# Performance work log

Hardware: AMD Instinct MI355X
Metric: run time of the kernel (lower is better)

## Reference

```python
import jax, jax.numpy as jnp
import numpy as np

B, S, H = 8, 2048, 1024
NEG = 1.0e10


def setup_inputs() -> dict:
    key = jax.random.key(0)
    ks = jax.random.split(key, 9)
    scale = 1.0 / np.sqrt(H)
    x = jax.random.normal(ks[0], (B, S, H), dtype=jnp.float32)
    Wq = jax.random.normal(ks[1], (H, H), dtype=jnp.float32) * scale
    bq = jnp.zeros((H,), dtype=jnp.float32)
    Wk = jax.random.normal(ks[2], (H, H), dtype=jnp.float32) * scale
    bk = jnp.zeros((H,), dtype=jnp.float32)
    Wv = jax.random.normal(ks[3], (H, H), dtype=jnp.float32) * scale
    bv = jnp.zeros((H,), dtype=jnp.float32)
    gamma = jnp.ones((H,), dtype=jnp.float32)
    beta = jnp.zeros((H,), dtype=jnp.float32)
    return {"x": x, "Wq": Wq, "bq": bq, "Wk": Wk, "bk": bk,
            "Wv": Wv, "bv": bv, "gamma": gamma, "beta": beta}


def _layernorm(y, gamma, beta, eps=1e-5):
    mu = jnp.mean(y, axis=-1, keepdims=True)
    var = jnp.var(y, axis=-1, keepdims=True)
    return (y - mu) * jax.lax.rsqrt(var + eps) * gamma + beta


def reference(x, Wq, bq, Wk, bk, Wv, bv, gamma, beta):
    # QKV projections (single head, no 1/sqrt(d) scaling, per original code)
    q = x @ Wq + bq                       # [B, S, H]
    k = x @ Wk + bk                       # [B, S, H]
    v = x @ Wv + bv                       # [B, S, H]
    scores = jnp.einsum('bsh,bth->bst', q, k)   # [B, S, S]
    # non-standard multiplicative-subtractive causal mask
    mask = jnp.tril(jnp.ones((S, S), dtype=scores.dtype))  # [S, S]
    scores = scores * mask - NEG * (1.0 - mask)
    probs = jax.nn.softmax(scores, axis=-1)
    attn = jnp.einsum('bst,bth->bsh', probs, v)
    return _layernorm(v + attn, gamma, beta)
```

## Files before the change

### kernel.cpp

```cpp
#include <hip/hip_runtime.h>

#define SQ 2048
#define HD 1024
#define NB 8
#define NTOT (NB*SQ)
#define NT2 8
#define NTRI2 36
#define CE ((long long)NTRI2*65536)

typedef _Float16 f16x8 __attribute__((ext_vector_type(8)));
typedef float f32x4 __attribute__((ext_vector_type(4)));
typedef short s16x8 __attribute__((ext_vector_type(8)));
typedef unsigned short u16;

__device__ __forceinline__ u16 f2h(float x){
  _Float16 h = (_Float16)x;
  u16 u; __builtin_memcpy(&u, &h, 2); return u;
}

#define STG(gp, lp) __builtin_amdgcn_global_load_lds( \
    (const __attribute__((address_space(1))) unsigned*)(gp), \
    (__attribute__((address_space(3))) unsigned*)(lp), 16, 0, 0)

template<int EPI>
__global__ __launch_bounds__(512, 2)
void gemm8(const u16* __restrict__ A, const u16* __restrict__ B,
           float* Cf, u16* Ch, u16* Vt,
           const float* __restrict__ b0, const float* __restrict__ b1,
           const float* __restrict__ b2,
           int K, int lda, int ldb, int ldc,
           long long sA, long long sB, long long sC)
{
  const int z = blockIdx.z;
  int bi, bj, tri = 0;
  if (EPI == 1){
    int t = blockIdx.x;
    int i = (int)((sqrtf(8.f * (float)t + 1.f) - 1.f) * 0.5f);
    while ((i + 1) * (i + 2) / 2 <= t) ++i;
    while (i * (i + 1) / 2 > t) --i;
    bi = i;  bj = t - i * (i + 1) / 2;  tri = t;
  } else {
    bi = blockIdx.x;  bj = blockIdx.y;
    if (EPI == 2) tri = bi * (bi + 1) / 2;
  }

  __shared__ short lds[4 * 16384];

  const int tid  = threadIdx.x;
  const int lane = tid & 63, w = tid >> 6;
  const int wm2 = w >> 2, wn4 = w & 3;
  const int lrow = lane & 15, kgrp = lane >> 4;

  const long long rowA = (long long)bi * 256;
  const long long colB = (long long)bj * 256;

  const int rt = tid >> 3;
  const int qp = (tid & 7) ^ (rt & 7);
  const int kq = qp & 3;
  const int rh = (qp >> 2) << 7;

  const u16 *sAp[2], *sBp[2];
  if (EPI == 2){
    const u16* Pb = A + (long long)z * sA + (long long)tri * 65536;
    #pragma unroll
    for (int i = 0; i < 2; i++)
      sAp[i] = Pb + (i * 64 + rt + rh) * 256 + kq * 8;
  } else {
    const u16* Ab = A + (EPI == 0 ? 0LL : (long long)z * sA);
    #pragma unroll
    for (int i = 0; i < 2; i++)
      sAp[i] = Ab + (rowA + i * 64 + rt + rh) * (long long)lda + kq * 8;
  }
  {
    const u16* Bb = B + (long long)z * sB;
    #pragma unroll
    for (int i = 0; i < 2; i++)
      sBp[i] = Bb + (colB + i * 64 + rt + rh) * (long long)ldb + kq * 8;
  }

  const int aoff = lrow * 64 + ((((wm2 << 2) | kgrp) ^ (lrow & 7)) << 3);
  const int boff = 8192 + ((wn4 & 1) * 64 + lrow) * 64
                 + (((((wn4 >> 1) << 2) | kgrp) ^ (lrow & 7)) << 3);

  f32x4 acc[8][4];
  const f32x4 zf = {0.f, 0.f, 0.f, 0.f};
  #pragma unroll
  for (int m = 0; m < 8; m++)
    #pragma unroll
    for (int n = 0; n < 4; n++) acc[m][n] = zf;

  int KT = K >> 5;
  if (EPI == 2){ int t = (bi + 1) * 8; if (t < KT) KT = t; }

  auto stage = [&](int b){
    #pragma unroll
    for (int i = 0; i < 2; i++) STG(sAp[i], lds + b * 16384 +        (i * 8 + w) * 512);
    #pragma unroll
    for (int i = 0; i < 2; i++) STG(sBp[i], lds + b * 16384 + 8192 + (i * 8 + w) * 512);
  };
  auto advance = [&](int tS){
    long long advA = 32;
    if (EPI == 2) advA = ((tS & 7) == 7) ? (65536 - 224) : 32;
    sAp[0] += advA; sAp[1] += advA; sBp[0] += 32; sBp[1] += 32;
  };

  stage(0); advance(0);
  if (KT > 1){ stage(1); advance(1); }
  if (KT > 2){ stage(2); advance(2); }
  if (KT > 2)      { asm volatile("s_waitcnt vmcnt(8)" ::: "memory"); }
  else if (KT > 1) { asm volatile("s_waitcnt vmcnt(4)" ::: "memory"); }
  else             { asm volatile("s_waitcnt vmcnt(0)" ::: "memory"); }
  __builtin_amdgcn_s_barrier();

  for (int kt = 0; kt < KT; ++kt){
    const short* Ab = lds + (kt & 3) * 16384;
    if (kt + 3 < KT){ stage((kt + 3) & 3); advance(kt + 3); }

    f16x8 bfr[4], af[4];
    #pragma unroll
    for (int n = 0; n < 4; n++)
      bfr[n] = *(const f16x8*)(Ab + boff + n * 1024);
    #pragma unroll
    for (int m = 0; m < 4; m++)
      af[m] = *(const f16x8*)(Ab + aoff + m * 1024);

    __builtin_amdgcn_s_setprio(1);
    #pragma unroll
    for (int n = 0; n < 4; n++)
      #pragma unroll
      for (int m = 0; m < 4; m++)
        acc[m][n] = __builtin_amdgcn_mfma_f32_16x16x32_f16(af[m], bfr[n], acc[m][n], 0, 0, 0);
    __builtin_amdgcn_s_setprio(0);
    __builtin_amdgcn_s_barrier();

    #pragma unroll
    for (int m = 0; m < 4; m++)
      af[m] = *(const f16x8*)(Ab + aoff + (4 + m) * 1024);

    __builtin_amdgcn_s_setprio(1);
    #pragma unroll
    for (int n = 0; n < 4; n++)
      #pragma unroll
      for (int m = 0; m < 4; m++)
        acc[4 + m][n] = __builtin_amdgcn_mfma_f32_16x16x32_f16(af[m], bfr[n], acc[4 + m][n], 0, 0, 0);
    __builtin_amdgcn_s_setprio(0);

    const int rem = KT - 1 - kt;
    if (rem >= 3)      { asm volatile("s_waitcnt vmcnt(8)" ::: "memory"); }
    else if (rem == 2) { asm volatile("s_waitcnt vmcnt(4)" ::: "memory"); }
    else if (rem == 1) { asm volatile("s_waitcnt vmcnt(0)" ::: "memory"); }
    if (rem > 0) __builtin_amdgcn_s_barrier();
  }

  if (EPI == 0){
    if (z < 2){
      u16* c = Ch + (long long)z * sC;
      const float* bias = z ? b1 : b0;
      #pragma unroll
      for (int n = 0; n < 4; n++){
        int col = (int)colB + wn4 * 64 + n * 16 + lrow;
        float ba = bias[col];
        #pragma unroll
        for (int m = 0; m < 8; m++){
          long long r = rowA + wm2 * 128 + m * 16 + kgrp * 4;
          #pragma unroll
          for (int j = 0; j < 4; j++)
            c[(r + j) * ldc + col] = f2h(acc[m][n][j] + ba);
        }
      }
    } else {
      #pragma unroll
      for (int n = 0; n < 4; n++){
        int col = (int)colB + wn4 * 64 + n * 16 + lrow;
        float ba = b2[col];
        #pragma unroll
        for (int m = 0; m < 8; m++){
          long long r = rowA + wm2 * 128 + m * 16 + kgrp * 4;
          int bb = (int)(r >> 11);
          int s  = (int)(r & 2047);
          u16* vtc = Vt + ((long long)bb * HD + col) * SQ + s;
          #pragma unroll
          for (int j = 0; j < 4; j++){
            float v = acc[m][n][j] + ba;
            Cf[(r + j) * ldc + col] = v;
            vtc[j] = f2h(v);
          }
        }
      }
    }
  } else if (EPI == 1){
    float* cf = Cf + (long long)z * sC + (long long)tri * 65536;
    #pragma unroll
    for (int n = 0; n < 4; n++){
      int col = wn4 * 64 + n * 16 + lrow;
      #pragma unroll
      for (int m = 0; m < 8; m++){
        int r = wm2 * 128 + m * 16 + kgrp * 4;
        #pragma unroll
        for (int j = 0; j < 4; j++)
          cf[(r + j) * 256 + col] = acc[m][n][j];
      }
    }
  } else {
    float* cf = Cf + (long long)z * sC;
    #pragma unroll
    for (int n = 0; n < 4; n++){
      int col = (int)colB + wn4 * 64 + n * 16 + lrow;
      #pragma unroll
      for (int m = 0; m < 8; m++){
        long long r = rowA + wm2 * 128 + m * 16 + kgrp * 4;
        #pragma unroll
        for (int j = 0; j < 4; j++){
          long long o = (r + j) * ldc + col;
          cf[o] = acc[m][n][j] + cf[o];
        }
      }
    }
  }
}

__global__ __launch_bounds__(256)
void prep_x(const float* __restrict__ X, u16* __restrict__ Xh)
{
  const long long n8 = (long long)NTOT * HD / 8;
  for (long long i = (long long)blockIdx.x * 256 + threadIdx.x; i < n8;
       i += (long long)gridDim.x * 256){
    const float* p = X + i * 8;
    float4 a = *(const float4*)p;
    float4 b = *(const float4*)(p + 4);
    float f[8] = {a.x, a.y, a.z, a.w, b.x, b.y, b.z, b.w};
    s16x8 h;
    #pragma unroll
    for (int j = 0; j < 8; j++) h[j] = (short)f2h(f[j]);
    *(s16x8*)&Xh[i * 8] = h;
  }
}

__global__ void prep_w(const float* __restrict__ Wq, const float* __restrict__ Wk,
                       const float* __restrict__ Wv, u16* __restrict__ Wt)
{
  __shared__ float t[32][33];
  const float* Win = (blockIdx.z == 0) ? Wq : (blockIdx.z == 1) ? Wk : Wv;
  const size_t zo = (size_t)blockIdx.z * HD * HD;
  int n0 = blockIdx.x * 32, k0 = blockIdx.y * 32;
  int tx = threadIdx.x, ty = threadIdx.y;
  #pragma unroll
  for (int i = 0; i < 4; i++)
    t[ty + 8*i][tx] = Win[(size_t)(k0 + ty + 8*i) * HD + n0 + tx];
  __syncthreads();
  #pragma unroll
  for (int i = 0; i < 4; i++)
    Wt[zo + (size_t)(n0 + ty + 8*i) * HD + k0 + tx] = f2h(t[tx][ty + 8*i]);
}

__global__ __launch_bounds__(256)
void softmax_causal(const float* __restrict__ SC, u16* __restrict__ P)
{
  const int s = blockIdx.x;
  const int i = s >> 8;
  const int tri = i * (i + 1) / 2;
  const long long base = (long long)blockIdx.y * CE + (long long)tri * 65536
                       + (long long)(s & 255) * 256;
  const float* scb = SC + base;
  u16* pb = P + base;

  __shared__ float buf[SQ];
  __shared__ float red[4];
  const int tid = threadIdx.x, lane = tid & 63, wid = tid >> 6;

  float m = -3.4e38f;
  for (int t = tid; t <= s; t += 256){
    float v = scb[(t >> 8) * 65536 + (t & 255)];
    buf[t] = v; m = fmaxf(m, v);
  }
  #pragma unroll
  for (int o = 32; o; o >>= 1) m = fmaxf(m, __shfl_xor(m, o));
  if (lane == 0) red[wid] = m;
  __syncthreads();
  m = fmaxf(fmaxf(red[0], red[1]), fmaxf(red[2], red[3]));
  __syncthreads();

  float sum = 0.f;
  for (int t = tid; t <= s; t += 256){ float e = __expf(buf[t] - m); buf[t] = e; sum += e; }
  #pragma unroll
  for (int o = 32; o; o >>= 1) sum += __shfl_xor(sum, o);
  if (lane == 0) red[wid] = sum;
  __syncthreads();
  sum = red[0] + red[1] + red[2] + red[3];
  const float inv = 1.f / sum;

  const int lim = (i + 1) << 8;
  for (int t = tid; t < lim; t += 256)
    pb[(t >> 8) * 65536 + (t & 255)] = (t <= s) ? f2h(buf[t] * inv) : (u16)0;
}

__global__ __launch_bounds__(256)
void layernorm_inplace(float* __restrict__ Y, const float* __restrict__ gamma,
                       const float* __restrict__ beta)
{
  float* y = Y + (long long)blockIdx.x * HD;
  const int tid = threadIdx.x, lane = tid & 63, wid = tid >> 6;
  float xv[4];
  float s = 0.f, ss = 0.f;
  #pragma unroll
  for (int i = 0; i < 4; i++){
    float v = y[tid + i * 256];
    xv[i] = v; s += v; ss += v * v;
  }
  #pragma unroll
  for (int o = 32; o; o >>= 1){ s += __shfl_xor(s, o); ss += __shfl_xor(ss, o); }
  __shared__ float r1[4], r2[4];
  if (lane == 0){ r1[wid] = s; r2[wid] = ss; }
  __syncthreads();
  s  = r1[0] + r1[1] + r1[2] + r1[3];
  ss = r2[0] + r2[1] + r2[2] + r2[3];
  const float mu   = s * (1.f / HD);
  const float var  = ss * (1.f / HD) - mu * mu;
  const float rstd = rsqrtf(var + 1e-5f);
  #pragma unroll
  for (int i = 0; i < 4; i++){
    int c = tid + i * 256;
    y[c] = (xv[i] - mu) * rstd * gamma[c] + beta[c];
  }
}

extern "C" void kernel_launch(void* const* d_in, const int* in_sizes, int n_in,
                              void* d_out, int out_size, void* d_ws, size_t ws_size,
                              hipStream_t stream)
{
  const float* x     = (const float*)d_in[0];
  const float* Wq    = (const float*)d_in[1];
  const float* bq    = (const float*)d_in[2];
  const float* Wk    = (const float*)d_in[3];
  const float* bk    = (const float*)d_in[4];
  const float* Wv    = (const float*)d_in[5];
  const float* bv    = (const float*)d_in[6];
  const float* gamma = (const float*)d_in[7];
  const float* beta  = (const float*)d_in[8];
  float* out = (float*)d_out;

  char* wsp = (char*)d_ws;
  size_t off = 0;
  auto alloc = [&](size_t bytes) -> char* {
    char* p = wsp + off;
    off = (off + bytes + 255) & ~(size_t)255;
    return p;
  };

  u16* Wt = (u16*)alloc(3ULL * HD * HD * 2);
  u16* QK = (u16*)alloc(2ULL * NTOT * HD * 2);
  u16* Vt = (u16*)alloc((size_t)NB * HD * SQ * 2);

  size_t rem = (ws_size > off) ? (ws_size - off) : 0;
  size_t perb = (size_t)CE * 6;
  int G = (int)(rem / perb);
  if (G > NB) G = NB;
  if (G < 1)  G = 1;
  u16*   xh = (u16*)(wsp + off);
  float* SC = (float*)(wsp + off);
  u16*   P  = (u16*)(wsp + off + (size_t)G * CE * 4);

  u16* Qh = QK;
  u16* Kh = QK + (size_t)NTOT * HD;
  float* V = out;

  prep_x<<<dim3(2048), dim3(256), 0, stream>>>(x, xh);
  prep_w<<<dim3(HD/32, HD/32, 3), dim3(32, 8), 0, stream>>>(Wq, Wk, Wv, Wt);

  gemm8<0><<<dim3(NTOT/256, HD/256, 3), 512, 0, stream>>>(
      xh, Wt, V, QK, Vt, bq, bk, bv,
      HD, HD, HD, HD,
      0LL, (long long)HD * HD, (long long)NTOT * HD);

  for (int g0 = 0; g0 < NB; g0 += G){
    int g = (G < NB - g0) ? G : (NB - g0);
    gemm8<1><<<dim3(NTRI2, 1, g), 512, 0, stream>>>(
        Qh + (size_t)g0 * SQ * HD, Kh + (size_t)g0 * SQ * HD,
        SC, nullptr, nullptr, nullptr, nullptr, nullptr,
        HD, HD, HD, 256,
        (long long)SQ * HD, (long long)SQ * HD, CE);
    softmax_causal<<<dim3(SQ, g), 256, 0, stream>>>(SC, P);
    gemm8<2><<<dim3(NT2, HD/256, g), 512, 0, stream>>>(
        P, Vt + (size_t)g0 * HD * SQ,
        out + (size_t)g0 * SQ * HD, nullptr, nullptr, nullptr, nullptr, nullptr,
        SQ, 256, SQ, HD,
        CE, (long long)HD * SQ, (long long)SQ * HD);
  }

  layernorm_inplace<<<dim3(NTOT), 256, 0, stream>>>(out, gamma, beta);
}
```

Before: 396.9 us.

## Split GEMM k-step into four MFMA quadrants interleaved with LDS reads and global prefetch

Restructures the inner GEMM loop into four 4x2 MFMA quadrant phases, reusing A and B fragments across phases. LDS fragment reads and the global-to-LDS prefetch issues are spread between phases, with sched_barriers, s_barriers and lgkmcnt waits separating them. The aim is to overlap LDS and global traffic with MFMA work in a ping-pong style schedule. In exchange it adds several more workgroup barriers per k-step, which could add stall time, and it keeps fewer fragment registers live at once.

```diff
diff --git a/kernel.cpp b/kernel.cpp
--- a/kernel.cpp
+++ b/kernel.cpp
@@ -66,10 +66,10 @@
     for (int i = 0; i < 2; i++)
       sAp[i] = Pb + (i * 64 + rt + rh) * 256 + kq * 8;
   } else {
-    const u16* Ab = A + (EPI == 0 ? 0LL : (long long)z * sA);
+    const u16* Ab0 = A + (EPI == 0 ? 0LL : (long long)z * sA);
     #pragma unroll
     for (int i = 0; i < 2; i++)
-      sAp[i] = Ab + (rowA + i * 64 + rt + rh) * (long long)lda + kq * 8;
+      sAp[i] = Ab0 + (rowA + i * 64 + rt + rh) * (long long)lda + kq * 8;
   }
   {
     const u16* Bb = B + (long long)z * sB;
@@ -114,35 +114,73 @@
 
   for (int kt = 0; kt < KT; ++kt){
     const short* Ab = lds + (kt & 3) * 16384;
-    if (kt + 3 < KT){ stage((kt + 3) & 3); advance(kt + 3); }
-
-    f16x8 bfr[4], af[4];
-    #pragma unroll
-    for (int n = 0; n < 4; n++)
-      bfr[n] = *(const f16x8*)(Ab + boff + n * 1024);
-    #pragma unroll
-    for (int m = 0; m < 4; m++)
-      af[m] = *(const f16x8*)(Ab + aoff + m * 1024);
-
+    const bool pf = (kt + 3 < KT);
+    const int nb = (kt + 3) & 3;
+
+    f16x8 af[4], bn0[2], bn1[2];
+
+    #pragma unroll
+    for (int m = 0; m < 4; m++) af[m] = *(const f16x8*)(Ab + aoff + m * 1024);
+    #pragma unroll
+    for (int n = 0; n < 2; n++) bn0[n] = *(const f16x8*)(Ab + boff + n * 1024);
+    if (pf){
+      STG(sAp[0], lds + nb * 16384 + (0 * 8 + w) * 512);
+      STG(sAp[1], lds + nb * 16384 + (1 * 8 + w) * 512);
+    }
+    __builtin_amdgcn_sched_barrier(0);
+    __builtin_amdgcn_s_barrier();
+    asm volatile("s_waitcnt lgkmcnt(0)" ::: "memory");
+    __builtin_amdgcn_sched_barrier(0);
     __builtin_amdgcn_s_setprio(1);
     #pragma unroll
-    for (int n = 0; n < 4; n++)
+    for (int n = 0; n < 2; n++)
       #pragma unroll
       for (int m = 0; m < 4; m++)
-        acc[m][n] = __builtin_amdgcn_mfma_f32_16x16x32_f16(af[m], bfr[n], acc[m][n], 0, 0, 0);
+        acc[m][n] = __builtin_amdgcn_mfma_f32_16x16x32_f16(af[m], bn0[n], acc[m][n], 0, 0, 0);
     __builtin_amdgcn_s_setprio(0);
     __builtin_amdgcn_s_barrier();
 
     #pragma unroll
-    for (int m = 0; m < 4; m++)
-      af[m] = *(const f16x8*)(Ab + aoff + (4 + m) * 1024);
-
+    for (int n = 0; n < 2; n++) bn1[n] = *(const f16x8*)(Ab + boff + (2 + n) * 1024);
+    if (pf){
+      STG(sBp[0], lds + nb * 16384 + 8192 + (0 * 8 + w) * 512);
+      STG(sBp[1], lds + nb * 16384 + 8192 + (1 * 8 + w) * 512);
+      advance(kt + 3);
+    }
+    __builtin_amdgcn_sched_barrier(0);
+    __builtin_amdgcn_s_barrier();
+    asm volatile("s_waitcnt lgkmcnt(0)" ::: "memory");
+    __builtin_amdgcn_sched_barrier(0);
     __builtin_amdgcn_s_setprio(1);
     #pragma unroll
-    for (int n = 0; n < 4; n++)
+    for (int n = 0; n < 2; n++)
       #pragma unroll
       for (int m = 0; m < 4; m++)
-        acc[4 + m][n] = __builtin_amdgcn_mfma_f32_16x16x32_f16(af[m], bfr[n], acc[4 + m][n], 0, 0, 0);
+        acc[m][2 + n] = __builtin_amdgcn_mfma_f32_16x16x32_f16(af[m], bn1[n], acc[m][2 + n], 0, 0, 0);
+    __builtin_amdgcn_s_setprio(0);
+    __builtin_amdgcn_s_barrier();
+
+    #pragma unroll
+    for (int m = 0; m < 4; m++) af[m] = *(const f16x8*)(Ab + aoff + (4 + m) * 1024);
+    __builtin_amdgcn_sched_barrier(0);
+    __builtin_amdgcn_s_barrier();
+    asm volatile("s_waitcnt lgkmcnt(0)" ::: "memory");
+    __builtin_amdgcn_sched_barrier(0);
+    __builtin_amdgcn_s_setprio(1);
+    #pragma unroll
+    for (int n = 0; n < 2; n++)
+      #pragma unroll
+      for (int m = 0; m < 4; m++)
+        acc[4 + m][2 + n] = __builtin_amdgcn_mfma_f32_16x16x32_f16(af[m], bn1[n], acc[4 + m][2 + n], 0, 0, 0);
+    __builtin_amdgcn_s_setprio(0);
+    __builtin_amdgcn_s_barrier();
+
+    __builtin_amdgcn_s_setprio(1);
+    #pragma unroll
+    for (int n = 0; n < 2; n++)
+      #pragma unroll
+      for (int m = 0; m < 4; m++)
+        acc[4 + m][n] = __builtin_amdgcn_mfma_f32_16x16x32_f16(af[m], bn0[n], acc[4 + m][n], 0, 0, 0);
     __builtin_amdgcn_s_setprio(0);
 
     const int rem = KT - 1 - kt;
```

Result: no change. 391.8 us (-1.3%).
